# Optimization experiments

Measured on AMD Instinct MI355X. Metric: run time of the kernel, lower is better.

## Reference

```python
import jax, jax.numpy as jnp
import numpy as np

B, V, M, H, T = 512, 256, 128, 512, 16  # batch, vocab, memory_size, hidden_dim, timing_dim
ALPHA = 0.95


def setup_inputs() -> dict:
    key = jax.random.key(0)
    ks = jax.random.split(key, 8)
    return {
        "x": jax.random.uniform(ks[0], (B, V), dtype=jnp.float32),
        "memory": jax.random.normal(ks[1], (B, M, V), dtype=jnp.float32),
        "memory_timings": jax.random.randint(ks[2], (B, M), 0, 1000, dtype=jnp.int64) if jax.config.jax_enable_x64 else jax.random.randint(ks[2], (B, M), 0, 1000).astype(jnp.int32),
        "memory_surprise": jax.random.uniform(ks[3], (B, M), dtype=jnp.float32),
        "last_prediction": jax.random.uniform(ks[4], (B, V), dtype=jnp.float32),
        "W1": jax.random.normal(ks[5], (V * M + M * T, H), dtype=jnp.float32) * 0.01,
        "b1": jnp.zeros((H,), dtype=jnp.float32),
        "W2": jax.random.normal(ks[6], (H, V), dtype=jnp.float32) * 0.01,
        "b2": jnp.zeros((V,), dtype=jnp.float32),
    }


def reference(x, memory, memory_timings, memory_surprise, last_prediction, W1, b1, W2, b2):
    b = x.shape[0]
    ar = jnp.arange(b)
    # compute_surprise
    surprise = -jnp.sum(x * jnp.log(last_prediction + 1e-6), axis=1)  # [B]
    # update_memory_timings
    timings = memory_timings + 1
    msurp = memory_surprise * ALPHA
    # update_memory: argmin-scatter into memory/timings/surprise
    idx = jnp.argmin(msurp, axis=1)  # [B]
    memory = memory.at[ar, idx].set(x)
    timings = timings.at[ar, idx].set(0)
    msurp = msurp.at[ar, idx].set(surprise)
    # compute_prediction: sort by timing, gather-reorder memory
    order = jnp.argsort(timings, axis=1)  # stable ascending, [B, M]
    sorted_t = jnp.take_along_axis(timings, order, axis=1)  # [B, M]
    sorted_mem = jnp.take_along_axis(memory, order[:, :, None], axis=1)  # [B, M, V]
    # binary encoding of timings: (t // 2**k) % 2 for k in [0, T)
    bits = ((sorted_t[:, :, None] >> jnp.arange(T)) & 1).astype(jnp.float32)  # [B, M, T]
    pred_in = jnp.concatenate([sorted_mem.reshape(b, -1), bits.reshape(b, -1)], axis=1)
    h = jax.nn.relu(pred_in @ W1 + b1)
    return h @ W2 + b2
```

## Files before the change

kernel.cpp:

```cpp
#include <hip/hip_runtime.h>

typedef unsigned int uint;
typedef unsigned short ushort;
typedef __attribute__((ext_vector_type(8))) short short8;
typedef __attribute__((ext_vector_type(4))) float f32x4;

#define B_   512
#define V_   256
#define M_   128
#define H_   512
#define T_   16
#define KTOT 34816

__device__ __forceinline__ ushort f2bf(float f) {
  uint u = __builtin_bit_cast(uint, f);
  u += 0x7fffu + ((u >> 16) & 1u);
  return (ushort)(u >> 16);
}

__device__ __forceinline__ int swz_k(int k, int row) {
  return (k & ~31) | (((((k >> 3) & 3) ^ ((row >> 1) & 3)) << 3)) | (k & 7);
}

__global__ __launch_bounds__(256) void prep_kernel(
    const float* __restrict__ x, const float* __restrict__ mem,
    const int* __restrict__ timings, const float* __restrict__ msurp,
    const float* __restrict__ b1,
    ushort* __restrict__ A, float* __restrict__ h_pre)
{
  const int b = blockIdx.x, tid = threadIdx.x;
  __shared__ int s_t[M_];
  __shared__ int s_row[M_];
  __shared__ int s_st[M_];
  __shared__ int s_idx;

  if (tid < 64) {
    float v0 = msurp[b * M_ + tid];
    float v1 = msurp[b * M_ + tid + 64];
    float v; int i;
    if (v1 < v0) { v = v1; i = tid + 64; } else { v = v0; i = tid; }
    #pragma unroll
    for (int off = 32; off > 0; off >>= 1) {
      float ov = __shfl_down(v, off);
      int   oi = __shfl_down(i, off);
      if (ov < v || (ov == v && oi < i)) { v = ov; i = oi; }
    }
    if (tid == 0) s_idx = i;
  }
  __syncthreads();
  const int idx = s_idx;

  if (tid < M_) {
    int t = timings[b * M_ + tid] + 1;
    if (tid == idx) t = 0;
    s_t[tid] = t;
  }
  h_pre[(size_t)b * H_ + tid]       = b1[tid];
  h_pre[(size_t)b * H_ + 256 + tid] = b1[256 + tid];
  __syncthreads();

  if (tid < M_) {
    const int t = s_t[tid];
    int r = 0;
    for (int j = 0; j < M_; ++j) {
      int tj = s_t[j];
      r += (tj < t || (tj == t && j < tid)) ? 1 : 0;
    }
    s_row[r] = tid;
    s_st[r]  = t;
  }
  __syncthreads();

  if (tid < M_) {
    const int t = s_st[tid];
    uint p[8];
    #pragma unroll
    for (int h = 0; h < 8; ++h) {
      uint lo = ((t >> (2 * h)) & 1) ? 0x3F80u : 0u;
      uint hi = ((t >> (2 * h + 1)) & 1) ? 0x3F80u : 0u;
      p[h] = lo | (hi << 16);
    }
    const int k0 = V_ * M_ + tid * T_;
    uint4 w0; w0.x = p[0]; w0.y = p[1]; w0.z = p[2]; w0.w = p[3];
    uint4 w1; w1.x = p[4]; w1.y = p[5]; w1.z = p[6]; w1.w = p[7];
    *(uint4*)(A + (size_t)b * KTOT + swz_k(k0, b))     = w0;
    *(uint4*)(A + (size_t)b * KTOT + swz_k(k0 + 8, b)) = w1;
  }

  const int lane = tid & 63, sub = tid >> 6;
  for (int it = 0; it < 32; ++it) {
    const int slot = it * 4 + sub;
    const int rowm = s_row[slot];
    const float* src = (rowm == idx) ? (x + (size_t)b * V_)
                                     : (mem + ((size_t)b * M_ + rowm) * V_);
    f32x4 v = *(const f32x4*)(src + lane * 4);
    uint2 o;
    o.x = (uint)f2bf(v[0]) | ((uint)f2bf(v[1]) << 16);
    o.y = (uint)f2bf(v[2]) | ((uint)f2bf(v[3]) << 16);
    const int k = slot * V_ + lane * 4;
    *(uint2*)(A + (size_t)b * KTOT + swz_k(k, b)) = o;
  }
}

#define BM 256
#define BN 128
#define SPLITK 32
#define KCH 1088
#define NCHU 34

#define GLD16(g, l) __builtin_amdgcn_global_load_lds( \
  (const __attribute__((address_space(1))) void*)(g), \
  (__attribute__((address_space(3))) void*)(l), 16, 0, 0)

template<bool USE_ATOMIC>
__global__ __launch_bounds__(512) void gemm1_kernel(
    const ushort* __restrict__ A, const float* __restrict__ W1,
    float* __restrict__ dst)
{
  __shared__ __align__(16) ushort As[2][BM * 32];
  __shared__ __align__(16) ushort Bs[2][BN * 32];

  const int bid  = blockIdx.x;
  const int tile = bid & 7;
  const int sk   = bid >> 3;
  const int b0   = (tile >> 2) * BM;
  const int n0   = (tile & 3) * BN;
  const int tid  = threadIdx.x, wave = tid >> 6, lane = tid & 63;
  const int wm   = wave >> 1;
  const int wn   = wave & 1;
  const long kb0 = (long)sk * KCH;

  f32x4 acc[4][4];
  #pragma unroll
  for (int i = 0; i < 4; ++i)
    #pragma unroll
    for (int j = 0; j < 4; ++j) acc[i][j] = (f32x4)0.f;

  const int ar  = wave * 32 + (lane >> 2);
  const int akk = (lane & 3) * 8;
  auto stageA = [&](int buf, long kb) {
    GLD16(A + ((size_t)(b0 + ar))      * KTOT + kb + akk, &As[buf][(wave * 32) * 32]);
    GLD16(A + ((size_t)(b0 + ar + 16)) * KTOT + kb + akk, &As[buf][(wave * 32 + 16) * 32]);
  };

  const int bn_  = tid & 127;
  const int bkc  = tid >> 7;
  const float* w1p = W1 + (size_t)(kb0 + bkc * 8) * H_ + n0 + bn_;
  ushort* bdst0 = &Bs[0][bn_ * 32 + ((bkc ^ ((bn_ >> 1) & 3)) * 8)];
  ushort* bdst1 = &Bs[1][bn_ * 32 + ((bkc ^ ((bn_ >> 1) & 3)) * 8)];

  float br[8];
  auto loadB = [&](float* r, int c) {
    const float* p = w1p + (size_t)c * 32 * H_;
    #pragma unroll
    for (int i = 0; i < 8; ++i) r[i] = p[(size_t)i * H_];
  };
  auto writeB = [&](const float* r, ushort* d) {
    uint4 o;
    o.x = (uint)f2bf(r[0]) | ((uint)f2bf(r[1]) << 16);
    o.y = (uint)f2bf(r[2]) | ((uint)f2bf(r[3]) << 16);
    o.z = (uint)f2bf(r[4]) | ((uint)f2bf(r[5]) << 16);
    o.w = (uint)f2bf(r[6]) | ((uint)f2bf(r[7]) << 16);
    *(uint4*)d = o;
  };

  const int xo = (((lane >> 4) ^ ((lane >> 1) & 3)) * 8);

  stageA(0, kb0);
  loadB(br, 0);
  writeB(br, bdst0);
  __syncthreads();

  for (int c = 0; c < NCHU; ++c) {
    const int cur = c & 1;
    float br2[8];
    if (c + 1 < NCHU) {
      loadB(br2, c + 1);
      stageA(cur ^ 1, kb0 + (long)(c + 1) * 32);
    }
    const ushort* as = &As[cur][(wm * 64 + (lane & 15)) * 32 + xo];
    const ushort* bs = &Bs[cur][(wn * 64 + (lane & 15)) * 32 + xo];
    short8 af[4], bf[4];
    #pragma unroll
    for (int i = 0; i < 4; ++i) {
      af[i] = *(const short8*)(as + i * 16 * 32);
      bf[i] = *(const short8*)(bs + i * 16 * 32);
    }
    #pragma unroll
    for (int i = 0; i < 4; ++i)
      #pragma unroll
      for (int j = 0; j < 4; ++j)
        acc[i][j] = __builtin_amdgcn_mfma_f32_16x16x32_bf16(af[i], bf[j], acc[i][j], 0, 0, 0);
    if (c + 1 < NCHU)
      writeB(br2, cur ? bdst0 : bdst1);
    __syncthreads();
  }

  const int row0 = b0 + wm * 64 + (lane >> 4) * 4;
  const int col0 = n0 + wn * 64 + (lane & 15);
  if constexpr (USE_ATOMIC) {
    #pragma unroll
    for (int i = 0; i < 4; ++i)
      #pragma unroll
      for (int j = 0; j < 4; ++j)
        #pragma unroll
        for (int r = 0; r < 4; ++r)
          atomicAdd(&dst[(size_t)(row0 + i * 16 + r) * H_ + col0 + j * 16], acc[i][j][r]);
  } else {
    float* P = dst + (size_t)sk * (B_ * H_);
    #pragma unroll
    for (int i = 0; i < 4; ++i)
      #pragma unroll
      for (int j = 0; j < 4; ++j)
        #pragma unroll
        for (int r = 0; r < 4; ++r)
          P[(size_t)(row0 + i * 16 + r) * H_ + col0 + j * 16] = acc[i][j][r];
  }
}

template<bool FROM_PARTIALS>
__global__ __launch_bounds__(256) void gemm2_kernel(
    const float* __restrict__ Pin, const float* __restrict__ b1,
    const float* __restrict__ W2, const float* __restrict__ b2,
    float* __restrict__ out)
{
  const int bb = blockIdx.x * 2;
  const int v  = threadIdx.x;
  __shared__ float hs[2][H_];

  {
    const int id  = v * 4;
    const int row = id >> 9, col = id & 511;
    f32x4 s;
    if constexpr (FROM_PARTIALS) {
      s = *(const f32x4*)(b1 + col);
      #pragma unroll 4
      for (int sk = 0; sk < SPLITK; ++sk)
        s += *(const f32x4*)(Pin + (size_t)sk * (B_ * H_) + (size_t)(bb + row) * H_ + col);
    } else {
      s = *(const f32x4*)(Pin + (size_t)(bb + row) * H_ + col);
    }
    f32x4 r;
    #pragma unroll
    for (int t = 0; t < 4; ++t) r[t] = fmaxf(s[t], 0.f);
    *(f32x4*)&hs[row][col] = r;
  }
  __syncthreads();

  float a0 = 0.f, a1 = 0.f;
  for (int j4 = 0; j4 < H_ / 4; ++j4) {
    f32x4 h0 = *(const f32x4*)&hs[0][j4 * 4];
    f32x4 h1 = *(const f32x4*)&hs[1][j4 * 4];
    #pragma unroll
    for (int t = 0; t < 4; ++t) {
      float w = W2[(size_t)(j4 * 4 + t) * V_ + v];
      a0 += h0[t] * w; a1 += h1[t] * w;
    }
  }
  const float bias = b2[v];
  out[(size_t)(bb + 0) * V_ + v] = a0 + bias;
  out[(size_t)(bb + 1) * V_ + v] = a1 + bias;
}

extern "C" void kernel_launch(void* const* d_in, const int* in_sizes, int n_in,
                              void* d_out, int out_size, void* d_ws, size_t ws_size,
                              hipStream_t stream) {
  const float* x   = (const float*)d_in[0];
  const float* mem = (const float*)d_in[1];
  const int*   tim = (const int*)d_in[2];
  const float* msu = (const float*)d_in[3];
  const float* W1  = (const float*)d_in[5];
  const float* b1  = (const float*)d_in[6];
  const float* W2  = (const float*)d_in[7];
  const float* b2  = (const float*)d_in[8];
  float* out = (float*)d_out;

  char* ws = (char*)d_ws;
  const size_t abytes = (size_t)B_ * KTOT * 2;
  const size_t pbytes = (size_t)SPLITK * B_ * H_ * 4;
  const size_t hbytes = (size_t)B_ * H_ * 4;
  const bool partials = ws_size >= abytes + pbytes + hbytes;

  ushort* A_ws  = (ushort*)ws;
  float*  P     = (float*)(ws + abytes);
  float*  h_pre = partials ? (float*)(ws + abytes + pbytes)
                           : (float*)(ws + abytes);

  prep_kernel<<<B_, 256, 0, stream>>>(x, mem, tim, msu, b1, A_ws, h_pre);
  if (partials) {
    gemm1_kernel<false><<<8 * SPLITK, 512, 0, stream>>>(A_ws, W1, P);
    gemm2_kernel<true><<<B_ / 2, 256, 0, stream>>>(P, b1, W2, b2, out);
  } else {
    gemm1_kernel<true><<<8 * SPLITK, 512, 0, stream>>>(A_ws, W1, h_pre);
    gemm2_kernel<false><<<B_ / 2, 256, 0, stream>>>(h_pre, b1, W2, b2, out);
  }
}
```

Before: 91.90 us.

## Deepen GEMM1 pipeline to triple-buffered A with explicit waitcnt and double split-K

Doubles the split-K factor so each block handles half as many K chunks. The A tile ring grows to three LDS buffers and loads are issued two chunks ahead, with manual s_waitcnt vmcnt and barriers in an unrolled macro loop so the VMEM queue is not fully drained each iteration. Launch bounds now request 4 blocks per CU. The risks are a larger split-K partial reduction or more atomics, more LDS per block, and fragile hand-counted vmcnt values.

Result: slower. 103.4 us (+12.5%).

```diff
diff --git a/kernel.cpp b/kernel.cpp
--- a/kernel.cpp
+++ b/kernel.cpp
@@ -104,20 +104,20 @@
 
 #define BM 256
 #define BN 128
-#define SPLITK 32
-#define KCH 1088
-#define NCHU 34
+#define SPLITK 64
+#define KCH 544
+#define NCHU 17
 
 #define GLD16(g, l) __builtin_amdgcn_global_load_lds( \
   (const __attribute__((address_space(1))) void*)(g), \
   (__attribute__((address_space(3))) void*)(l), 16, 0, 0)
 
 template<bool USE_ATOMIC>
-__global__ __launch_bounds__(512) void gemm1_kernel(
+__global__ __launch_bounds__(512, 4) void gemm1_kernel(
     const ushort* __restrict__ A, const float* __restrict__ W1,
     float* __restrict__ dst)
 {
-  __shared__ __align__(16) ushort As[2][BM * 32];
+  __shared__ __align__(16) ushort As[3][BM * 32];
   __shared__ __align__(16) ushort Bs[2][BN * 32];
 
   const int bid  = blockIdx.x;
@@ -138,7 +138,8 @@
 
   const int ar  = wave * 32 + (lane >> 2);
   const int akk = (lane & 3) * 8;
-  auto stageA = [&](int buf, long kb) {
+  auto stageA = [&](int buf, int chunk) {
+    const long kb = kb0 + (long)chunk * 32;
     GLD16(A + ((size_t)(b0 + ar))      * KTOT + kb + akk, &As[buf][(wave * 32) * 32]);
     GLD16(A + ((size_t)(b0 + ar + 16)) * KTOT + kb + akk, &As[buf][(wave * 32 + 16) * 32]);
   };
@@ -146,10 +147,8 @@
   const int bn_  = tid & 127;
   const int bkc  = tid >> 7;
   const float* w1p = W1 + (size_t)(kb0 + bkc * 8) * H_ + n0 + bn_;
-  ushort* bdst0 = &Bs[0][bn_ * 32 + ((bkc ^ ((bn_ >> 1) & 3)) * 8)];
-  ushort* bdst1 = &Bs[1][bn_ * 32 + ((bkc ^ ((bn_ >> 1) & 3)) * 8)];
-
-  float br[8];
+  const int b_woff = bn_ * 32 + ((bkc ^ ((bn_ >> 1) & 3)) * 8);
+
   auto loadB = [&](float* r, int c) {
     const float* p = w1p + (size_t)c * 32 * H_;
     #pragma unroll
@@ -164,37 +163,45 @@
     *(uint4*)d = o;
   };
 
-  const int xo = (((lane >> 4) ^ ((lane >> 1) & 3)) * 8);
-
-  stageA(0, kb0);
-  loadB(br, 0);
-  writeB(br, bdst0);
-  __syncthreads();
-
-  for (int c = 0; c < NCHU; ++c) {
-    const int cur = c & 1;
-    float br2[8];
-    if (c + 1 < NCHU) {
-      loadB(br2, c + 1);
-      stageA(cur ^ 1, kb0 + (long)(c + 1) * 32);
-    }
-    const ushort* as = &As[cur][(wm * 64 + (lane & 15)) * 32 + xo];
-    const ushort* bs = &Bs[cur][(wn * 64 + (lane & 15)) * 32 + xo];
-    short8 af[4], bf[4];
-    #pragma unroll
-    for (int i = 0; i < 4; ++i) {
-      af[i] = *(const short8*)(as + i * 16 * 32);
-      bf[i] = *(const short8*)(bs + i * 16 * 32);
-    }
-    #pragma unroll
-    for (int i = 0; i < 4; ++i)
-      #pragma unroll
-      for (int j = 0; j < 4; ++j)
-        acc[i][j] = __builtin_amdgcn_mfma_f32_16x16x32_bf16(af[i], bf[j], acc[i][j], 0, 0, 0);
-    if (c + 1 < NCHU)
-      writeB(br2, cur ? bdst0 : bdst1);
-    __syncthreads();
-  }
+  const int xo     = (((lane >> 4) ^ ((lane >> 1) & 3)) * 8);
+  const int a_roff = (wm * 64 + (lane & 15)) * 32;
+  const int b_roff = (wn * 64 + (lane & 15)) * 32;
+
+  float brE[8], brO[8];
+
+#define GITER(c, BRL, BRW, ISSUE, WRITE, VMC) do {                            \
+    asm volatile("s_waitcnt vmcnt(" VMC ") lgkmcnt(0)" ::: "memory");         \
+    __builtin_amdgcn_s_barrier();                                             \
+    __builtin_amdgcn_sched_barrier(0);                                        \
+    if (ISSUE) { loadB(BRL, (c) + 2); stageA(((c) + 2) % 3, (c) + 2); }       \
+    const ushort* as_ = &As[(c) % 3][a_roff + xo];                            \
+    const ushort* bs_ = &Bs[(c) & 1][b_roff + xo];                            \
+    short8 af[4], bf[4];                                                      \
+    _Pragma("unroll") for (int i = 0; i < 4; ++i) {                           \
+      af[i] = *(const short8*)(as_ + i * 16 * 32);                            \
+      bf[i] = *(const short8*)(bs_ + i * 16 * 32); }                          \
+    _Pragma("unroll") for (int i = 0; i < 4; ++i)                             \
+      _Pragma("unroll") for (int j = 0; j < 4; ++j)                           \
+        acc[i][j] = __builtin_amdgcn_mfma_f32_16x16x32_bf16(af[i], bf[j],     \
+                                                            acc[i][j], 0,0,0);\
+    if (WRITE) writeB(BRW, &Bs[((c) + 1) & 1][b_woff]);                       \
+  } while (0)
+
+  loadB(brE, 0);
+  stageA(0, 0);
+  loadB(brO, 1);
+  stageA(1, 1);
+  writeB(brE, &Bs[0][b_woff]);
+
+  #pragma unroll 1
+  for (int cc = 0; cc < 14; cc += 2) {
+    GITER(cc,     brE, brO, true, true, "10");
+    GITER(cc + 1, brO, brE, true, true, "10");
+  }
+  GITER(14, brE, brO, true,  true,  "10");
+  GITER(15, brO, brE, false, true,  "10");
+  GITER(16, brE, brO, false, false, "0");
+#undef GITER
 
   const int row0 = b0 + wm * 64 + (lane >> 4) * 4;
   const int col0 = n0 + wn * 64 + (lane & 15);
```
